# Kernel optimization log

Hardware: AMD Instinct MI355X
Metric: run time of the kernel (lower is better)

The kernel has to match this reference:

```python
import jax, jax.numpy as jnp
import numpy as np

HEADS, K = 8, 7

def setup_inputs() -> dict:
    key = jax.random.key(0)
    ks = jax.random.split(key, 8)
    C = 432
    B, H, W = 1, 56, 56
    n = lambda k, s, std: jax.random.normal(k, s, dtype=jnp.float32) * std
    return {
        "x": n(ks[0], (B, H, W, C), 1.0),
        "qkv_w": n(ks[1], (3 * C, C), 0.02),
        "qkv_b": jnp.zeros((3 * C,), jnp.float32),
        "rpb": n(ks[2], (HEADS, 2 * K - 1, 2 * K - 1), 0.02),
        "conv1_w": n(ks[3], (C, C // 54, K, K), 0.05),   # grouped conv, groups=54 -> 8 in-ch per group
        "conv1_b": jnp.zeros((C,), jnp.float32),
        "conv2_w": n(ks[4], (K * K * HEADS, C, 1, 1), 0.05),
        "conv2_b": jnp.zeros((K * K * HEADS,), jnp.float32),
        "ghost_head": n(ks[5], (C, K, K), 0.02),
        "proj2_w": n(ks[6], (C, 2 * C), 0.02),
        "proj2_b": jnp.zeros((C,), jnp.float32),
    }

def _nat_indices(L, K):
    i = jnp.arange(L)
    ni = jnp.clip(i - K // 2, 0, L - K)                      # clamped window start (NAT semantics)
    idx = ni[:, None] + jnp.arange(K)[None, :]               # [L,K] neighbor coords
    rpb_idx = (K - 1) - (i - ni)[:, None] + jnp.arange(K)[None, :]  # [L,K] rpb lookup
    return idx, rpb_idx

def reference(x, qkv_w, qkv_b, rpb, conv1_w, conv1_b, conv2_w, conv2_b, ghost_head, proj2_w, proj2_b):
    B, H, W, C = x.shape
    hd = C // HEADS
    scale = hd ** -0.5
    qkv = (x @ qkv_w.T + qkv_b).reshape(B, H, W, 3, HEADS, hd)
    qkv = jnp.transpose(qkv, (3, 0, 4, 1, 2, 5))             # [3,B,heads,H,W,hd]
    q, k, v = qkv[0], qkv[1], qkv[2]
    q = q * scale
    idx_i, rpb_i = _nat_indices(H, K)
    idx_j, rpb_j = _nat_indices(W, K)
    ii = idx_i[:, None, :, None]                             # [H,1,K,1]
    jj = idx_j[None, :, None, :]                             # [1,W,1,K]
    # ---- NAT QK + RPB ----
    k_nbr = k[:, :, ii, jj, :]                               # [B,heads,H,W,K,K,hd]
    attn = jnp.einsum('bghwd,bghwuvd->bghwuv', q, k_nbr)
    bias = rpb[:, rpb_i[:, None, :, None], rpb_j[None, :, None, :]]  # [heads,H,W,K,K]
    attn = (attn + bias[None]).reshape(B, HEADS, H, W, K * K)
    attn = jax.nn.softmax(attn, axis=-1)
    # ---- Hadamard conv-attention branch ----
    to_nchw = lambda t: jnp.transpose(t, (0, 2, 3, 1, 4)).reshape(B, H, W, C).transpose(0, 3, 1, 2)
    had = to_nchw(q) * to_nchw(k) * scale                    # note: q already scaled once (faithful)
    h = jax.lax.conv_general_dilated(had, conv1_w, (1, 1), ((K // 2, K // 2), (K // 2, K // 2)),
                                     feature_group_count=54,
                                     dimension_numbers=('NCHW', 'OIHW', 'NCHW')) + conv1_b[None, :, None, None]
    h = jax.nn.gelu(h, approximate=False)
    h = jax.lax.conv_general_dilated(h, conv2_w, (1, 1), ((0, 0), (0, 0)),
                                     dimension_numbers=('NCHW', 'OIHW', 'NCHW')) + conv2_b[None, :, None, None]
    h = jax.nn.softmax(h, axis=1)                            # softmax over all heads*K*K channels
    h_attn = jnp.transpose(h, (0, 2, 3, 1)).reshape(B, H, W, HEADS, K * K).transpose(0, 3, 1, 2, 4)
    attn_A = jnp.concatenate([attn, h_attn], axis=-1)        # [B,heads,H,W,2*K*K]
    # ---- ELSA ghost-head local aggregation (zero-padded centered window, lam=0, gamma=1) ----
    v_tmp = to_nchw(v)                                       # [B,C,H,W]
    a_tmp = jnp.transpose(attn_A, (0, 2, 3, 1, 4)).reshape(B, H, W, -1).transpose(0, 3, 1, 2)
    G = 2 * HEADS                                            # 2*K*K slots per head -> 2*heads attn groups
    a_g = a_tmp.reshape(B, G, K * K, H, W)
    vp = jnp.pad(v_tmp, ((0, 0), (0, 0), (K // 2, K // 2), (K // 2, K // 2)))
    pi = jnp.arange(H)[:, None] + jnp.arange(K)[None, :]     # [H,K]
    pj = jnp.arange(W)[:, None] + jnp.arange(K)[None, :]
    patches = vp[:, :, pi[:, None, :, None], pj[None, :, None, :]].reshape(B, C, H, W, K * K)
    elsa = jnp.einsum('bgchwk,bgkhw->bgchw',
                      patches.reshape(B, G, C // G, H, W, K * K), a_g).reshape(B, C, H, W)
    elsa = elsa + jnp.einsum('bchwk,ck->bchw', patches, ghost_head.reshape(C, K * K))
    attn_tmp = jnp.transpose(elsa, (0, 2, 3, 1)).reshape(B, H, W, HEADS, hd).transpose(0, 3, 1, 2, 4)
    # ---- NAT AV over fused attention (both 49-slot halves share the NAT neighborhood) ----
    a2 = (attn_A[..., :K * K] + attn_A[..., K * K:]).reshape(B, HEADS, H, W, K, K)
    v_nbr = v[:, :, ii, jj, :]                               # [B,heads,H,W,K,K,hd]
    av = jnp.einsum('bghwuv,bghwuvd->bghwd', a2, v_nbr)
    out = jnp.concatenate([av, attn_tmp], axis=-1)           # [B,heads,H,W,2*hd]
    out = jnp.transpose(out, (0, 2, 3, 1, 4)).reshape(B, H, W, 2 * C)
    return out @ proj2_w.T + proj2_b
```

## Files before the change

### kernel.cpp

```cpp
#include <hip/hip_runtime.h>
#include <hip/hip_bf16.h>
#include <math.h>

#define N_PIX 3136
#define CDIM 432
#define NHEADS 8
#define HD 54
#define KK 49
#define C2 392

typedef __attribute__((ext_vector_type(8))) short bf16x8;
typedef __attribute__((ext_vector_type(4))) float f32x4;
typedef __attribute__((ext_vector_type(8))) unsigned short ushort8;

__device__ __forceinline__ void gload_lds16(const void* g, void* l) {
    __builtin_amdgcn_global_load_lds(
        (const __attribute__((address_space(1))) void*)g,
        (__attribute__((address_space(3))) void*)l, 16, 0, 0);
}

__device__ __forceinline__ unsigned short f2bf(float f) {
    __hip_bfloat16 b = __float2bfloat16(f);
    unsigned short u;
    __builtin_memcpy(&u, &b, 2);
    return u;
}

__device__ __forceinline__ size_t perm_off(int r, int k, int Kp) {
    int p = ((k >> 3) & 7) ^ (r & 7);
    return (size_t)r * Kp + ((k >> 6) << 6) + (p << 3) + (k & 7);
}

__device__ __forceinline__ void convert_body(
    const float* __restrict__ src, __hip_bfloat16* __restrict__ dst,
    int Mlog, int Mpad, int Klog, int Kp, int id)
{
    int chunks = Kp >> 3;
    if (id >= Mpad * chunks) return;
    int r = id / chunks, cb = id % chunks;
    int k0 = cb << 3;
    __hip_bfloat16 vv[8];
    #pragma unroll
    for (int e = 0; e < 8; e++) {
        int k = k0 + e;
        float f = (r < Mlog && k < Klog) ? src[(size_t)r * Klog + k] : 0.f;
        vv[e] = __float2bfloat16(f);
    }
    int p = (cb & 7) ^ (r & 7);
    __hip_bfloat16* d = dst + (size_t)r * Kp + ((cb >> 3) << 6) + (p << 3);
    *(ushort8*)d = *(const ushort8*)vv;
}

__global__ __launch_bounds__(256) void prep_kernel(
    const float* __restrict__ x, const float* __restrict__ qkv_w,
    const float* __restrict__ conv2_w, const float* __restrict__ proj2_w,
    const float* __restrict__ ghost,
    __hip_bfloat16* __restrict__ xb, __hip_bfloat16* __restrict__ qkvwb,
    __hip_bfloat16* __restrict__ c2wb, __hip_bfloat16* __restrict__ p2wb,
    float* __restrict__ ghostT)
{
    int b = blockIdx.x;
    if (b < 83) {
        int id = b * 256 + threadIdx.x;
        if (id < CDIM * KK) {
            int cc = id / KK, t = id % KK;
            ghostT[t * CDIM + cc] = ghost[id];
        }
    } else if (b < 769) {
        convert_body(x, xb, 3136, 3136, 432, 448, (b - 83) * 256 + threadIdx.x);
    } else if (b < 1063) {
        convert_body(qkv_w, qkvwb, 1296, 1344, 432, 448, (b - 769) * 256 + threadIdx.x);
    } else if (b < 1161) {
        convert_body(conv2_w, c2wb, 392, 448, 432, 448, (b - 1063) * 256 + threadIdx.x);
    } else {
        convert_body(proj2_w, p2wb, 432, 448, 864, 896, (b - 1161) * 256 + threadIdx.x);
    }
}

__global__ __launch_bounds__(256) void gemm_mfma(
    const __hip_bfloat16* __restrict__ A, const __hip_bfloat16* __restrict__ B,
    const float* __restrict__ bias,
    float* __restrict__ O0, float* __restrict__ O1,
    __hip_bfloat16* __restrict__ VB,
    int Nlog, int Kp, int mode, float qscale, int ldO)
{
    __shared__ __hip_bfloat16 lA[64 * 64];
    __shared__ __hip_bfloat16 lB[64 * 64];
    const int tid = threadIdx.x;
    const int w = tid >> 6, lane = tid & 63;
    const int row0 = blockIdx.y * 64, col0 = blockIdx.x * 64;
    const int wr = (w >> 1) * 32, wc = (w & 1) * 32;
    const int srow = lane >> 3, schk = lane & 7;
    f32x4 acc[2][2] = {};

    for (int k0 = 0; k0 < Kp; k0 += 64) {
        #pragma unroll
        for (int t = 0; t < 2; t++) {
            int lid = w * 2 + t;
            const __hip_bfloat16* ga =
                A + (size_t)(row0 + lid * 8 + srow) * Kp + k0 + schk * 8;
            gload_lds16(ga, &lA[lid * 8 * 64]);
            const __hip_bfloat16* gb =
                B + (size_t)(col0 + lid * 8 + srow) * Kp + k0 + schk * 8;
            gload_lds16(gb, &lB[lid * 8 * 64]);
        }
        __syncthreads();
        #pragma unroll
        for (int ks = 0; ks < 2; ks++) {
            bf16x8 af[2], bfr[2];
            int c = ks * 4 + (lane >> 4);
            #pragma unroll
            for (int mi = 0; mi < 2; mi++) {
                int ra = wr + mi * 16 + (lane & 15);
                af[mi] = *(const bf16x8*)&lA[ra * 64 + ((c ^ (ra & 7)) << 3)];
                int rb = wc + mi * 16 + (lane & 15);
                bfr[mi] = *(const bf16x8*)&lB[rb * 64 + ((c ^ (rb & 7)) << 3)];
            }
            #pragma unroll
            for (int mi = 0; mi < 2; mi++)
                #pragma unroll
                for (int ni = 0; ni < 2; ni++)
                    acc[mi][ni] = __builtin_amdgcn_mfma_f32_16x16x32_bf16(
                        af[mi], bfr[ni], acc[mi][ni], 0, 0, 0);
        }
        __syncthreads();
    }

    #pragma unroll
    for (int mi = 0; mi < 2; mi++) {
        #pragma unroll
        for (int ni = 0; ni < 2; ni++) {
            #pragma unroll
            for (int rr = 0; rr < 4; rr++) {
                int r = row0 + wr + mi * 16 + (lane >> 4) * 4 + rr;
                int cc = col0 + wc + ni * 16 + (lane & 15);
                if (cc >= Nlog) continue;
                float val = acc[mi][ni][rr] + bias[cc];
                if (mode == 0) {
                    int s = cc / CDIM, cch = cc - s * CDIM;
                    if (s == 0) {
                        O0[(size_t)r * CDIM + cch] = val * qscale;
                    } else if (s == 1) {
                        O1[(size_t)r * CDIM + cch] = val;
                    } else {
                        int hh = cch / HD, dd = cch - hh * HD;
                        VB[((size_t)hh * N_PIX + r) * 64 + dd] =
                            __float2bfloat16(val);
                    }
                } else {
                    O0[(size_t)r * ldO + cc] = val;
                }
            }
        }
    }
}

__global__ __launch_bounds__(256) void attn_kernel(
    const float* __restrict__ q, const float* __restrict__ k,
    const float* __restrict__ rpb, float* __restrict__ attn)
{
    int bid = blockIdx.x;
    int nb = (bid & 7) * 784 + (bid >> 3);
    int wave = nb * 4 + (threadIdx.x >> 6);
    wave = __builtin_amdgcn_readfirstlane(wave);
    int lane = threadIdx.x & 63;
    int h = wave / N_PIX;
    int n = wave - h * N_PIX;
    int i = n / 56, j = n % 56;
    int ni = min(max(i - 3, 0), 49), nj = min(max(j - 3, 0), 49);
    int t = lane, u = t / 7, v = t % 7;
    float logit = -1e30f;
    if (t < KK) {
        int nb2 = (ni + u) * 56 + (nj + v);
        const float2* qp = (const float2*)(q + (size_t)n * CDIM + h * HD);
        const float2* kp = (const float2*)(k + (size_t)nb2 * CDIM + h * HD);
        float s = 0.f;
        #pragma unroll
        for (int d = 0; d < HD / 2; d++) {
            float2 qv = qp[d], kv = kp[d];
            s += qv.x * kv.x + qv.y * kv.y;
        }
        int ri = 6 - (i - ni) + u;
        int rj = 6 - (j - nj) + v;
        logit = s + rpb[h * 169 + ri * 13 + rj];
    }
    float m = logit;
    #pragma unroll
    for (int off = 32; off; off >>= 1) m = fmaxf(m, __shfl_xor(m, off));
    float e = (t < KK) ? expf(logit - m) : 0.f;
    float ssum = e;
    #pragma unroll
    for (int off = 32; off; off >>= 1) ssum += __shfl_xor(ssum, off);
    if (t < KK) attn[(size_t)n * C2 + h * KK + t] = e / ssum;
}

#define TH 4
__global__ __launch_bounds__(256) void conv1_gelu_v2(
    const float* __restrict__ q, const float* __restrict__ k,
    const float* __restrict__ w, const float* __restrict__ b,
    __hip_bfloat16* __restrict__ out, float scale)
{
    int g = blockIdx.x % 54;
    int rt = blockIdx.x / 54;
    int r0 = rt * TH;
    int tid = threadIdx.x;
    int waveid = tid >> 6, lane = tid & 63;
    int ic = lane >> 3, oc = lane & 7;

    __shared__ float smem[10][8][68];

    float* sflat = &smem[0][0][0];
    for (int i = tid; i < 10 * 8 * 68; i += 256) sflat[i] = 0.f;

    float wreg[49];
    {
        const float* wp = w + ((size_t)(g * 8 + oc) * 8 + ic) * 49;
        #pragma unroll
        for (int t = 0; t < 49; t++) wreg[t] = wp[t];
    }
    __syncthreads();

    {
        int lic = tid & 7;
        int lpj = (tid >> 3) & 31;
        for (int rr = 0; rr < 10; rr++) {
            int pi = r0 - 3 + rr;
            if (pi < 0 || pi >= 56) continue;
            #pragma unroll
            for (int p0 = 0; p0 < 56; p0 += 32) {
                int pj = p0 + lpj;
                if (pj < 56) {
                    size_t off = (size_t)(pi * 56 + pj) * CDIM + g * 8 + lic;
                    smem[rr][lic][pj + 3] = q[off] * k[off] * scale;
                }
            }
        }
    }
    __syncthreads();

    int r = r0 + waveid;
    float bias_o = b[g * 8 + oc];
    for (int j0 = 0; j0 < 56; j0 += 4) {
        float acc0 = 0.f, acc1 = 0.f, acc2 = 0.f, acc3 = 0.f;
        #pragma unroll
        for (int u = 0; u < 7; u++) {
            const float* rp = &smem[waveid + u][ic][j0];
            float4 c0 = *(const float4*)(rp);
            float4 c1 = *(const float4*)(rp + 4);
            float4 c2 = *(const float4*)(rp + 8);
            float col[12] = {c0.x, c0.y, c0.z, c0.w,
                             c1.x, c1.y, c1.z, c1.w,
                             c2.x, c2.y, c2.z, c2.w};
            #pragma unroll
            for (int v = 0; v < 7; v++) {
                float wv = wreg[u * 7 + v];
                acc0 += wv * col[v + 0];
                acc1 += wv * col[v + 1];
                acc2 += wv * col[v + 2];
                acc3 += wv * col[v + 3];
            }
        }
        float accs[4] = {acc0, acc1, acc2, acc3};
        #pragma unroll
        for (int jj = 0; jj < 4; jj++) {
            float s = accs[jj];
            s += __shfl_xor(s, 8);
            s += __shfl_xor(s, 16);
            s += __shfl_xor(s, 32);
            accs[jj] = s;
        }
        if (ic == 0) {
            #pragma unroll
            for (int jj = 0; jj < 4; jj++) {
                float a = accs[jj] + bias_o;
                float gl = 0.5f * a * (1.0f + erff(a * 0.70710678118654752f));
                int n = r * 56 + j0 + jj;
                int kch = g * 8 + oc;
                out[perm_off(n, kch, 448)] = __float2bfloat16(gl);
            }
        }
    }
}

__global__ __launch_bounds__(128) void softmax_pack(
    const float* __restrict__ h2, const float* __restrict__ attn,
    unsigned* __restrict__ pk)
{
    __shared__ float red[128];
    int n = blockIdx.x, tid = threadIdx.x;
    const float* row = h2 + (size_t)n * C2;
    float m = -1e30f;
    float rv[4];
    #pragma unroll
    for (int idx = 0; idx < 4; idx++) {
        int c = tid + idx * 128;
        rv[idx] = (c < C2) ? row[c] : -1e30f;
        m = fmaxf(m, rv[idx]);
    }
    red[tid] = m; __syncthreads();
    for (int s = 64; s; s >>= 1) {
        if (tid < s) red[tid] = fmaxf(red[tid], red[tid + s]);
        __syncthreads();
    }
    m = red[0]; __syncthreads();
    float loc = 0.f;
    #pragma unroll
    for (int idx = 0; idx < 4; idx++) {
        int c = tid + idx * 128;
        if (c < C2) { rv[idx] = expf(rv[idx] - m); loc += rv[idx]; }
    }
    red[tid] = loc; __syncthreads();
    for (int s = 64; s; s >>= 1) {
        if (tid < s) red[tid] += red[tid + s];
        __syncthreads();
    }
    float inv = 1.0f / red[0];
    #pragma unroll
    for (int idx = 0; idx < 4; idx++) {
        int c = tid + idx * 128;
        if (c < C2) {
            float hval = rv[idx] * inv;
            float a = attn[(size_t)n * C2 + c];
            int hh = c / KK, t = c - hh * KK;
            unsigned word = ((unsigned)f2bf(a) << 16) | (unsigned)f2bf(a + hval);
            pk[((size_t)n * 8 + hh) * 52 + t] = word;
        }
    }
}

__global__ __launch_bounds__(256) void combine_int(
    const __hip_bfloat16* __restrict__ vb, const unsigned* __restrict__ pk,
    const float* __restrict__ ghostT, __hip_bfloat16* __restrict__ comb)
{
    __shared__ float gs[KK * HD];
    int bid = blockIdx.x;
    int nb = (bid & 7) * 625 + (bid >> 3);
    int h = (nb * 4) / 2500;
    for (int f = threadIdx.x; f < KK * HD; f += 256) {
        int t = f / HD, dd = f - t * HD;
        gs[f] = ghostT[t * CDIM + h * HD + dd];
    }
    __syncthreads();

    int task = nb * 4 + (threadIdx.x >> 6);
    task = __builtin_amdgcn_readfirstlane(task);
    int lane = threadIdx.x & 63;
    int rem = task - h * 2500;
    int i = 3 + rem / 50;
    int j = 3 + (rem - (rem / 50) * 50);
    int n = i * 56 + j;
    int d = (lane < HD) ? lane : (HD - 1);
    bool lo = (d < 27);

    const unsigned* pkrow = pk + ((size_t)n * 8 + h) * 52;
    const __hip_bfloat16* vwin =
        vb + ((size_t)h * N_PIX + (i - 3) * 56 + (j - 3)) * 64 + d;

    float S_ah = 0.f, S_a = 0.f, S_g = 0.f;
    #pragma unroll
    for (int u = 0; u < 7; u++) {
        float vrow[7];
        #pragma unroll
        for (int vv = 0; vv < 7; vv++)
            vrow[vv] = __bfloat162float(vwin[(u * 56 + vv) * 64]);
        #pragma unroll
        for (int vv = 0; vv < 7; vv++) {
            const int t = u * 7 + vv;
            unsigned s = pkrow[t];
            float a  = __uint_as_float(s & 0xFFFF0000u);
            float ah = __uint_as_float(s << 16);
            float gt = gs[t * HD + d];
            S_ah += ah * vrow[vv];
            S_a  += a  * vrow[vv];
            S_g  += gt * vrow[vv];
        }
    }
    if (lane < HD) {
        float av = S_ah;
        float Sh = S_ah - S_a;
        float elsa = S_g + (lo ? S_a : Sh);
        comb[perm_off(n, h * 108 + d, 896)]      = __float2bfloat16(av);
        comb[perm_off(n, h * 108 + 54 + d, 896)] = __float2bfloat16(elsa);
    }
}

__global__ __launch_bounds__(256) void combine_bdr(
    const __hip_bfloat16* __restrict__ vb, const unsigned* __restrict__ pk,
    const float* __restrict__ ghostT, __hip_bfloat16* __restrict__ comb)
{
    __shared__ float gs[KK * HD];
    int bid = blockIdx.x;
    int nb = (bid & 7) * 159 + (bid >> 3);
    int h = (nb * 4) / 636;
    for (int f = threadIdx.x; f < KK * HD; f += 256) {
        int t = f / HD, dd = f - t * HD;
        gs[f] = ghostT[t * CDIM + h * HD + dd];
    }
    __syncthreads();

    int task = nb * 4 + (threadIdx.x >> 6);
    task = __builtin_amdgcn_readfirstlane(task);
    int lane = threadIdx.x & 63;
    int idx = task - h * 636;
    int i, j;
    if (idx < 336) {
        int r = idx / 56;
        i = (r < 3) ? r : 50 + r;
        j = idx - r * 56;
    } else {
        int idx2 = idx - 336;
        i = 3 + idx2 / 6;
        int jj = idx2 - (idx2 / 6) * 6;
        j = (jj < 3) ? jj : 50 + jj;
    }
    int n = i * 56 + j;
    int d = (lane < HD) ? lane : (HD - 1);
    bool lo = (d < 27);

    const unsigned* pkrow = pk + ((size_t)n * 8 + h) * 52;
    int ni = min(max(i - 3, 0), 49), nj = min(max(j - 3, 0), 49);
    const __hip_bfloat16* vhead = vb + (size_t)h * N_PIX * 64 + d;
    const __hip_bfloat16* vbc = vhead + (size_t)(ni * 56 + nj) * 64;

    float S_ahc = 0.f, S_ap = 0.f, S_ahp = 0.f, S_gp = 0.f;
    #pragma unroll
    for (int t = 0; t < KK; t++) {
        const int u = t / 7, vv = t % 7;
        unsigned s = pkrow[t];
        float a  = __uint_as_float(s & 0xFFFF0000u);
        float ah = __uint_as_float(s << 16);
        float vc = __bfloat162float(vbc[(u * 56 + vv) * 64]);
        S_ahc += ah * vc;
        int pi = i + u - 3, pj = j + vv - 3;
        if (pi >= 0 && pi < 56 && pj >= 0 && pj < 56) {
            float vp = __bfloat162float(vhead[(size_t)(pi * 56 + pj) * 64]);
            float gt = gs[t * HD + d];
            S_ahp += ah * vp; S_ap += a * vp; S_gp += gt * vp;
        }
    }
    if (lane < HD) {
        float av = S_ahc;
        float Shp = S_ahp - S_ap;
        float elsa = S_gp + (lo ? S_ap : Shp);
        comb[perm_off(n, h * 108 + d, 896)]      = __float2bfloat16(av);
        comb[perm_off(n, h * 108 + 54 + d, 896)] = __float2bfloat16(elsa);
    }
}

extern "C" void kernel_launch(void* const* d_in, const int* in_sizes, int n_in,
                              void* d_out, int out_size, void* d_ws, size_t ws_size,
                              hipStream_t stream)
{
    const float* x       = (const float*)d_in[0];
    const float* qkv_w   = (const float*)d_in[1];
    const float* qkv_b   = (const float*)d_in[2];
    const float* rpb     = (const float*)d_in[3];
    const float* conv1_w = (const float*)d_in[4];
    const float* conv1_b = (const float*)d_in[5];
    const float* conv2_w = (const float*)d_in[6];
    const float* conv2_b = (const float*)d_in[7];
    const float* ghost   = (const float*)d_in[8];
    const float* proj2_w = (const float*)d_in[9];
    const float* proj2_b = (const float*)d_in[10];
    float* out = (float*)d_out;

    float* ws = (float*)d_ws;
    const size_t NC = (size_t)N_PIX * CDIM;
    const size_t NA = (size_t)N_PIX * C2;
    float* q      = ws;
    float* k      = q + NC;
    float* attn   = k + NC;
    float* hat    = attn + NA;
    float* ghostT = hat + NA;
    unsigned* pk  = (unsigned*)(ghostT + 21168);
    __hip_bfloat16* bfbase = (__hip_bfloat16*)(pk + 1304576);
    __hip_bfloat16* xb     = bfbase;
    __hip_bfloat16* qkvwb  = xb    + (size_t)3136 * 448;
    __hip_bfloat16* c2wb   = qkvwb + (size_t)1344 * 448;
    __hip_bfloat16* p2wb   = c2wb  + (size_t)448 * 448;
    __hip_bfloat16* hb     = p2wb  + (size_t)448 * 896;
    __hip_bfloat16* cb     = hb    + (size_t)3136 * 448;
    __hip_bfloat16* vb16   = cb    + (size_t)3136 * 896;

    const float scale = 0.13608276348795434f;

    prep_kernel<<<1357, 256, 0, stream>>>(
        x, qkv_w, conv2_w, proj2_w, ghost, xb, qkvwb, c2wb, p2wb, ghostT);

    gemm_mfma<<<dim3(21, 49), 256, 0, stream>>>(
        xb, qkvwb, qkv_b, q, k, vb16, 1296, 448, 0, scale, 0);

    attn_kernel<<<(N_PIX * NHEADS) / 4, 256, 0, stream>>>(q, k, rpb, attn);

    conv1_gelu_v2<<<54 * 14, 256, 0, stream>>>(q, k, conv1_w, conv1_b, hb, scale);

    gemm_mfma<<<dim3(7, 49), 256, 0, stream>>>(
        hb, c2wb, conv2_b, hat, nullptr, nullptr, 392, 448, 1, 1.f, 392);

    softmax_pack<<<N_PIX, 128, 0, stream>>>(hat, attn, pk);

    combine_int<<<5000, 256, 0, stream>>>(vb16, pk, ghostT, cb);
    combine_bdr<<<1272, 256, 0, stream>>>(vb16, pk, ghostT, cb);

    gemm_mfma<<<dim3(7, 49), 256, 0, stream>>>(
        cb, p2wb, proj2_b, out, nullptr, nullptr, 432, 896, 1, 1.f, 432);
}
```

Measured before the change: 148.6 us.

## Compute NAT QK logits with bf16 MFMA over row-window blocks

Replaces the per-wave scalar fp32 QK dot product with a block-per-(head,row) kernel. It multiplies 64 query pixels against the 7-row key window (392+ keys) using bf16 MFMA, stages the scores in LDS, and then gathers the 49 neighbourhood logits for the softmax. The QKV GEMM epilogue now also writes head-major, zero-padded bf16 copies of Q and K, and the prep kernel zeroes the padding. This trades redundant MFMA work on out-of-window keys, plus extra bf16 writes, for far fewer scalar FLOPs and key reloads. It also lowers the logit precision to bf16.

```diff
diff --git a/kernel.cpp b/kernel.cpp
--- a/kernel.cpp
+++ b/kernel.cpp
@@ -3,6 +3,7 @@
 #include <math.h>
 
 #define N_PIX 3136
+#define NPAD 3200
 #define CDIM 432
 #define NHEADS 8
 #define HD 54
@@ -57,7 +58,7 @@
     const float* __restrict__ ghost,
     __hip_bfloat16* __restrict__ xb, __hip_bfloat16* __restrict__ qkvwb,
     __hip_bfloat16* __restrict__ c2wb, __hip_bfloat16* __restrict__ p2wb,
-    float* __restrict__ ghostT)
+    float* __restrict__ ghostT, __hip_bfloat16* __restrict__ qkzero)
 {
     int b = blockIdx.x;
     if (b < 83) {
@@ -72,8 +73,11 @@
         convert_body(qkv_w, qkvwb, 1296, 1344, 432, 448, (b - 769) * 256 + threadIdx.x);
     } else if (b < 1161) {
         convert_body(conv2_w, c2wb, 392, 448, 432, 448, (b - 1063) * 256 + threadIdx.x);
+    } else if (b < 1357) {
+        convert_body(proj2_w, p2wb, 432, 448, 864, 896, (b - 1161) * 256 + threadIdx.x);
     } else {
-        convert_body(proj2_w, p2wb, 432, 448, 864, 896, (b - 1161) * 256 + threadIdx.x);
+        int id = (b - 1357) * 256 + threadIdx.x;
+        if (id < 409600) ((ushort8*)qkzero)[id] = (ushort8)0;
     }
 }
 
@@ -82,6 +86,7 @@
     const float* __restrict__ bias,
     float* __restrict__ O0, float* __restrict__ O1,
     __hip_bfloat16* __restrict__ VB,
+    __hip_bfloat16* __restrict__ QB, __hip_bfloat16* __restrict__ KB,
     int Nlog, int Kp, int mode, float qscale, int ldO)
 {
     __shared__ __hip_bfloat16 lA[64 * 64];
@@ -138,14 +143,16 @@
                 float val = acc[mi][ni][rr] + bias[cc];
                 if (mode == 0) {
                     int s = cc / CDIM, cch = cc - s * CDIM;
+                    int hh = cch / HD, dd = cch - hh * HD;
                     if (s == 0) {
-                        O0[(size_t)r * CDIM + cch] = val * qscale;
+                        float qv = val * qscale;
+                        O0[(size_t)r * CDIM + cch] = qv;
+                        QB[((size_t)hh * NPAD + r) * 64 + dd] = __float2bfloat16(qv);
                     } else if (s == 1) {
                         O1[(size_t)r * CDIM + cch] = val;
+                        KB[((size_t)hh * NPAD + r) * 64 + dd] = __float2bfloat16(val);
                     } else {
-                        int hh = cch / HD, dd = cch - hh * HD;
-                        VB[((size_t)hh * N_PIX + r) * 64 + dd] =
-                            __float2bfloat16(val);
+                        VB[((size_t)hh * N_PIX + r) * 64 + dd] = __float2bfloat16(val);
                     }
                 } else {
                     O0[(size_t)r * ldO + cc] = val;
@@ -155,43 +162,68 @@
     }
 }
 
-__global__ __launch_bounds__(256) void attn_kernel(
-    const float* __restrict__ q, const float* __restrict__ k,
+__global__ __launch_bounds__(256) void attn_mfma(
+    const __hip_bfloat16* __restrict__ qb, const __hip_bfloat16* __restrict__ kb,
     const float* __restrict__ rpb, float* __restrict__ attn)
 {
+    __shared__ float Sl[16][404];
+    __shared__ float rpb_l[169];
     int bid = blockIdx.x;
-    int nb = (bid & 7) * 784 + (bid >> 3);
-    int wave = nb * 4 + (threadIdx.x >> 6);
-    wave = __builtin_amdgcn_readfirstlane(wave);
-    int lane = threadIdx.x & 63;
-    int h = wave / N_PIX;
-    int n = wave - h * N_PIX;
-    int i = n / 56, j = n % 56;
-    int ni = min(max(i - 3, 0), 49), nj = min(max(j - 3, 0), 49);
-    int t = lane, u = t / 7, v = t % 7;
-    float logit = -1e30f;
-    if (t < KK) {
-        int nb2 = (ni + u) * 56 + (nj + v);
-        const float2* qp = (const float2*)(q + (size_t)n * CDIM + h * HD);
-        const float2* kp = (const float2*)(k + (size_t)nb2 * CDIM + h * HD);
-        float s = 0.f;
-        #pragma unroll
-        for (int d = 0; d < HD / 2; d++) {
-            float2 qv = qp[d], kv = kp[d];
-            s += qv.x * kv.x + qv.y * kv.y;
-        }
-        int ri = 6 - (i - ni) + u;
-        int rj = 6 - (j - nj) + v;
-        logit = s + rpb[h * 169 + ri * 13 + rj];
-    }
-    float m = logit;
-    #pragma unroll
-    for (int off = 32; off; off >>= 1) m = fmaxf(m, __shfl_xor(m, off));
-    float e = (t < KK) ? expf(logit - m) : 0.f;
-    float ssum = e;
-    #pragma unroll
-    for (int off = 32; off; off >>= 1) ssum += __shfl_xor(ssum, off);
-    if (t < KK) attn[(size_t)n * C2 + h * KK + t] = e / ssum;
+    int nb = (bid & 7) * 56 + (bid >> 3);
+    int h = nb / 56, i = nb - (nb / 56) * 56;
+    int tid = threadIdx.x;
+    int w = tid >> 6, lane = tid & 63;
+    int l15 = lane & 15, l4 = lane >> 4;
+    int ni = min(max(i - 3, 0), 49);
+
+    for (int f = tid; f < 169; f += 256) rpb_l[f] = rpb[h * 169 + f];
+    __syncthreads();
+
+    const __hip_bfloat16* qrow = qb + ((size_t)h * NPAD + i * 56) * 64;
+    const __hip_bfloat16* kwin = kb + ((size_t)h * NPAD + ni * 56) * 64;
+
+    for (int rt = 0; rt < 4; rt++) {
+        bf16x8 af0 = *(const bf16x8*)(qrow + (size_t)(rt * 16 + l15) * 64 + l4 * 8);
+        bf16x8 af1 = *(const bf16x8*)(qrow + (size_t)(rt * 16 + l15) * 64 + 32 + l4 * 8);
+        for (int ct = w; ct < 25; ct += 4) {
+            bf16x8 b0 = *(const bf16x8*)(kwin + (size_t)(ct * 16 + l15) * 64 + l4 * 8);
+            bf16x8 b1 = *(const bf16x8*)(kwin + (size_t)(ct * 16 + l15) * 64 + 32 + l4 * 8);
+            f32x4 acc = {};
+            acc = __builtin_amdgcn_mfma_f32_16x16x32_bf16(af0, b0, acc, 0, 0, 0);
+            acc = __builtin_amdgcn_mfma_f32_16x16x32_bf16(af1, b1, acc, 0, 0, 0);
+            int col = ct * 16 + l15;
+            #pragma unroll
+            for (int r = 0; r < 4; r++)
+                Sl[l4 * 4 + r][col] = acc[r];
+        }
+        __syncthreads();
+        #pragma unroll
+        for (int pp = 0; pp < 4; pp++) {
+            int j = rt * 16 + w * 4 + pp;
+            if (j < 56) {
+                int n = i * 56 + j;
+                int nj = min(max(j - 3, 0), 49);
+                int t = lane;
+                float logit = -1e30f;
+                if (t < KK) {
+                    int u = t / 7, v = t - (t / 7) * 7;
+                    int col = u * 56 + nj + v;
+                    int ri = 6 - (i - ni) + u;
+                    int rj = 6 - (j - nj) + v;
+                    logit = Sl[j - rt * 16][col] + rpb_l[ri * 13 + rj];
+                }
+                float m = logit;
+                #pragma unroll
+                for (int off = 32; off; off >>= 1) m = fmaxf(m, __shfl_xor(m, off));
+                float e = (t < KK) ? expf(logit - m) : 0.f;
+                float ssum = e;
+                #pragma unroll
+                for (int off = 32; off; off >>= 1) ssum += __shfl_xor(ssum, off);
+                if (t < KK) attn[(size_t)n * C2 + h * KK + t] = e / ssum;
+            }
+        }
+        __syncthreads();
+    }
 }
 
 #define TH 4
@@ -481,21 +513,24 @@
     __hip_bfloat16* hb     = p2wb  + (size_t)448 * 896;
     __hip_bfloat16* cb     = hb    + (size_t)3136 * 448;
     __hip_bfloat16* vb16   = cb    + (size_t)3136 * 896;
+    __hip_bfloat16* qb16   = vb16  + (size_t)8 * N_PIX * 64;
+    __hip_bfloat16* kb16   = qb16  + (size_t)8 * NPAD * 64;
 
     const float scale = 0.13608276348795434f;
 
-    prep_kernel<<<1357, 256, 0, stream>>>(
-        x, qkv_w, conv2_w, proj2_w, ghost, xb, qkvwb, c2wb, p2wb, ghostT);
+    prep_kernel<<<2957, 256, 0, stream>>>(
+        x, qkv_w, conv2_w, proj2_w, ghost, xb, qkvwb, c2wb, p2wb, ghostT, qb16);
 
     gemm_mfma<<<dim3(21, 49), 256, 0, stream>>>(
-        xb, qkvwb, qkv_b, q, k, vb16, 1296, 448, 0, scale, 0);
-
-    attn_kernel<<<(N_PIX * NHEADS) / 4, 256, 0, stream>>>(q, k, rpb, attn);
+        xb, qkvwb, qkv_b, q, k, vb16, qb16, kb16, 1296, 448, 0, scale, 0);
+
+    attn_mfma<<<448, 256, 0, stream>>>(qb16, kb16, rpb, attn);
 
     conv1_gelu_v2<<<54 * 14, 256, 0, stream>>>(q, k, conv1_w, conv1_b, hb, scale);
 
     gemm_mfma<<<dim3(7, 49), 256, 0, stream>>>(
-        hb, c2wb, conv2_b, hat, nullptr, nullptr, 392, 448, 1, 1.f, 392);
+        hb, c2wb, conv2_b, hat, nullptr, nullptr, nullptr, nullptr,
+        392, 448, 1, 1.f, 392);
 
     softmax_pack<<<N_PIX, 128, 0, stream>>>(hat, attn, pk);
 
@@ -503,5 +538,6 @@
     combine_bdr<<<1272, 256, 0, stream>>>(vb16, pk, ghostT, cb);
 
     gemm_mfma<<<dim3(7, 49), 256, 0, stream>>>(
-        cb, p2wb, proj2_b, out, nullptr, nullptr, 432, 896, 1, 1.f, 432);
-}
+        cb, p2wb, proj2_b, out, nullptr, nullptr, nullptr, nullptr,
+        432, 896, 1, 1.f, 432);
+}
```

Result: no change. 151.2 us (+1.7%).
